# Kernel tuning notes

Hardware: AMD Instinct MI355X
Metric: run time of the kernel (lower is better)

Reference implementation:

```python
import jax, jax.numpy as jnp
import numpy as np

B, C, CO, N = 2, 32, 32, 64
MODES, LMAX, RBINS = 16, 2, 16
HALF = MODES // 2
NL = (LMAX + 1) ** 2  # 9 real spherical harmonics up to l=2
M = MODES ** 3
HID = 16  # round(CO * 0.5)


def _build_basis():
    # frequencies of the kept FNO corner modes along each axis
    f = np.concatenate([np.arange(HALF), np.arange(-HALF, 0)]).astype(np.float32)
    kx, ky, kz = np.meshgrid(f, f, f, indexing='ij')
    kx, ky, kz = kx.ravel(), ky.ravel(), kz.ravel()
    r = np.sqrt(kx ** 2 + ky ** 2 + kz ** 2)
    nzm = (r > 0).astype(np.float32)
    inv = np.where(r > 0, 1.0 / np.maximum(r, 1e-9), 0.0)
    ux, uy, uz = kx * inv, ky * inv, kz * inv
    # real spherical harmonics l=0,1,2 (cartesian form); all l>0 vanish at DC
    Y = np.stack([
        0.282095 * np.ones_like(r),
        0.488603 * uy, 0.488603 * uz, 0.488603 * ux,
        1.092548 * ux * uy, 1.092548 * uy * uz,
        0.315392 * (3.0 * uz ** 2 - nzm),
        1.092548 * ux * uz, 0.546274 * (ux ** 2 - uy ** 2)], axis=0)  # [NL, M]
    shell = np.minimum((r / (r.max() + 1e-6) * RBINS).astype(np.int64), RBINS - 1)
    cnt = np.bincount(shell, minlength=RBINS).astype(np.float32)
    w = 1.0 / np.sqrt(np.maximum(cnt, 1.0))
    mask = (shell[None, :] == np.arange(RBINS)[:, None]).astype(np.float32) * w[:, None]  # [RBINS, M]
    return (mask[:, None, :] * Y[None]).reshape(RBINS * NL, M).astype(np.float32)

BASIS = jnp.asarray(_build_basis())  # [K=144, M=4096], fixed projection basis
IDX = jnp.asarray(np.concatenate([np.arange(HALF), np.arange(N - HALF, N)]))  # kept mode indices


def cgelu(z):
    return jax.nn.gelu(z.real) + 1j * jax.nn.gelu(z.imag)


def setup_inputs() -> dict:
    key = jax.random.key(0)
    ks = jax.random.split(key, 17)
    rn = lambda k, s: jax.random.normal(k, s, dtype=jnp.float32)
    return {
        'x': rn(ks[0], (B, C, N, N, N)),
        'w_fno_r': rn(ks[1], (CO, C)) * 0.1, 'w_fno_i': rn(ks[2], (CO, C)) * 0.1,
        'b_fno_r': rn(ks[3], (CO,)) * 0.1, 'b_fno_i': rn(ks[4], (CO,)) * 0.1,
        'w_gate_r': rn(ks[5], (CO,)), 'w_gate_i': rn(ks[6], (CO,)),
        'w_spec_r': rn(ks[7], (RBINS, NL, C, CO)) * 0.1, 'w_spec_i': rn(ks[8], (RBINS, NL, C, CO)) * 0.1,
        'mlp_w1_r': rn(ks[9], (HID, CO)) * 0.1, 'mlp_w1_i': rn(ks[10], (HID, CO)) * 0.1,
        'mlp_b1_r': rn(ks[11], (HID,)) * 0.1, 'mlp_b1_i': rn(ks[12], (HID,)) * 0.1,
        'mlp_w2_r': rn(ks[13], (CO, HID)) * 0.1, 'mlp_w2_i': rn(ks[14], (CO, HID)) * 0.1,
        'mlp_b2_r': rn(ks[15], (CO,)) * 0.1, 'mlp_b2_i': rn(ks[16], (CO,)) * 0.1,
    }


def reference(x, w_fno_r, w_fno_i, b_fno_r, b_fno_i, w_gate_r, w_gate_i,
              w_spec_r, w_spec_i, mlp_w1_r, mlp_w1_i, mlp_b1_r, mlp_b1_i,
              mlp_w2_r, mlp_w2_i, mlp_b2_r, mlp_b2_i):
    cx = lambda r, i: (r + 1j * i).astype(jnp.complex64)
    xc = x.astype(jnp.complex64)
    w_fno, b_fno = cx(w_fno_r, w_fno_i), cx(b_fno_r, b_fno_i)
    w_gate = cx(w_gate_r, w_gate_i)
    w_spec = cx(w_spec_r, w_spec_i)
    w1, b1 = cx(mlp_w1_r, mlp_w1_i), cx(mlp_b1_r, mlp_b1_i)
    w2, b2 = cx(mlp_w2_r, mlp_w2_i), cx(mlp_b2_r, mlp_b2_i)

    # skip paths: complex 1x1-conv ('linear') and complex soft-gating
    skip_fno = jnp.einsum('oc,bcxyz->boxyz', w_fno, xc) + b_fno[None, :, None, None, None]
    skip_mlp = xc * w_gate[None, :, None, None, None]

    # Harmonic layer: FFT -> slice kept modes -> harmonic/radial projection
    # -> complex spectral conv -> inverse projection -> scatter -> iFFT
    xf = jnp.fft.fftn(xc, axes=(-3, -2, -1))
    xs = xf[:, :, IDX[:, None, None], IDX[None, :, None], IDX[None, None, :]].reshape(B, C, M)
    coeffs = jnp.einsum('bcm,km->bck', xs, BASIS).reshape(B, C, RBINS, NL)
    coeffs = jnp.einsum('bisl,slio->bosl', coeffs, w_spec)
    xs2 = jnp.einsum('bck,km->bcm', coeffs.reshape(B, CO, RBINS * NL), BASIS)
    full = jnp.zeros((B, CO, N, N, N), jnp.complex64).at[
        :, :, IDX[:, None, None], IDX[None, :, None], IDX[None, None, :]
    ].set(xs2.reshape(B, CO, MODES, MODES, MODES))
    x_fno = jnp.fft.ifftn(full, axes=(-3, -2, -1))

    x1 = x_fno + skip_fno  # n_layers=1 -> no activation here
    h = cgelu(jnp.einsum('hc,bcxyz->bhxyz', w1, x1) + b1[None, :, None, None, None])
    y = jnp.einsum('oh,bhxyz->boxyz', w2, h) + b2[None, :, None, None, None]
    return (y + skip_mlp).real
```

## Files before the change

kernel.cpp:

```cpp
#include <hip/hip_runtime.h>
#include <hip/hip_bf16.h>

#define PI2 6.283185307179586f

typedef __attribute__((ext_vector_type(8))) short short8;
typedef __attribute__((ext_vector_type(4))) float f32x4;

static const size_t O_Y      = 0;
static const size_t O_W1RT   = 36864;
static const size_t O_W1IT   = 37376;
static const size_t O_W1XR   = 37888;
static const size_t O_W1XI   = 38400;
static const size_t O_B1PR   = 38912;
static const size_t O_B1PI   = 38928;
static const size_t O_WSH    = 38944;
static const size_t O_SHELL  = 38960;
static const size_t O_ORDER  = 43056;
static const size_t O_SSTART = 47152;
static const size_t O_COEF   = 47232;
static const size_t O_COEF2  = 65664;
static const size_t O_XS     = 84096;
static const size_t O_FRAG   = 608384;
static const size_t O_T2     = 1132672;
static const size_t O_T1     = 3229824;

static __device__ __forceinline__ float geluf(float v) {
  float e = __expf(-1.702f * v);
  return v / (1.0f + e);
}

static __device__ __forceinline__ unsigned int f2bfbits(float f) {
  unsigned int u = __float_as_uint(f);
  u += 0x7fffu + ((u >> 16) & 1u);
  return u >> 16;
}

static __device__ __forceinline__ unsigned int pk2(float a, float b) {
  return f2bfbits(a) | (f2bfbits(b) << 16);
}

__global__ __launch_bounds__(256) void k0_init(
    const float* __restrict__ wfr, const float* __restrict__ wfi,
    const float* __restrict__ bfr, const float* __restrict__ bfi,
    const float* __restrict__ w1r, const float* __restrict__ w1i,
    const float* __restrict__ b1r, const float* __restrict__ b1i,
    const float* __restrict__ w2r, const float* __restrict__ w2i,
    float* __restrict__ ws) {
  float* Y    = ws + O_Y;
  float* w1rt = ws + O_W1RT;  float* w1it = ws + O_W1IT;
  float* W1xr = ws + O_W1XR;  float* W1xi = ws + O_W1XI;
  float* b1pr = ws + O_B1PR;  float* b1pi = ws + O_B1PI;
  float* wsh  = ws + O_WSH;
  int* shellOf = (int*)(ws + O_SHELL);
  int* order   = (int*)(ws + O_ORDER);
  int* sstart  = (int*)(ws + O_SSTART);

  __shared__ int cnt[16], fill[16], st[17];
  int tid = threadIdx.x;
  if (tid < 16) { cnt[tid] = 0; fill[tid] = 0; }
  __syncthreads();
  for (int m = tid; m < 4096; m += 256) {
    int ix = m >> 8, iy = (m >> 4) & 15, iz = m & 15;
    float kx = (float)(ix < 8 ? ix : ix - 16);
    float ky = (float)(iy < 8 ? iy : iy - 16);
    float kz = (float)(iz < 8 ? iz : iz - 16);
    float r2 = kx*kx + ky*ky + kz*kz;
    float r  = sqrtf(r2);
    float nzm = r2 > 0.f ? 1.f : 0.f;
    float inv = r2 > 0.f ? 1.0f / fmaxf(r, 1e-9f) : 0.f;
    float ux = kx*inv, uy = ky*inv, uz = kz*inv;
    Y[0*4096+m] = 0.282095f;
    Y[1*4096+m] = 0.488603f * uy;
    Y[2*4096+m] = 0.488603f * uz;
    Y[3*4096+m] = 0.488603f * ux;
    Y[4*4096+m] = 1.092548f * ux*uy;
    Y[5*4096+m] = 1.092548f * uy*uz;
    Y[6*4096+m] = 0.315392f * (3.0f*uz*uz - nzm);
    Y[7*4096+m] = 1.092548f * ux*uz;
    Y[8*4096+m] = 0.546274f * (ux*ux - uy*uy);
    float rmax = sqrtf(192.0f);
    float t = r / (rmax + 1e-6f) * 16.0f;
    int sh = (int)t; sh = sh > 15 ? 15 : sh;
    shellOf[m] = sh;
    atomicAdd(&cnt[sh], 1);
  }
  __syncthreads();
  if (tid == 0) { int a = 0; for (int s = 0; s < 16; ++s) { st[s] = a; a += cnt[s]; } st[16] = a; }
  __syncthreads();
  if (tid < 16) wsh[tid] = 1.0f / sqrtf(fmaxf((float)cnt[tid], 1.0f));
  if (tid < 17) sstart[tid] = st[tid];
  for (int m = tid; m < 4096; m += 256) {
    int sh = shellOf[m];
    int p = atomicAdd(&fill[sh], 1);
    order[st[sh] + p] = m;
  }
  for (int e = tid; e < 512; e += 256) {
    int j = e >> 5, c = e & 31;
    float ar = 0.f, ai = 0.f;
    for (int o = 0; o < 32; ++o) {
      float wr_ = w1r[j*32+o], wi_ = w1i[j*32+o];
      float fr  = wfr[o*32+c], fi_ = wfi[o*32+c];
      ar += wr_*fr - wi_*fi_;
      ai += wr_*fi_ + wi_*fr;
    }
    W1xr[c*16+j] = ar;  W1xi[c*16+j] = ai;
    w1rt[c*16+j] = w1r[j*32+c];
    w1it[c*16+j] = w1i[j*32+c];
  }
  if (tid < 16) {
    int j = tid;
    float ar = b1r[j], ai = b1i[j];
    for (int o = 0; o < 32; ++o) {
      ar += w1r[j*32+o]*bfr[o] - w1i[j*32+o]*bfi[o];
      ai += w1r[j*32+o]*bfi[o] + w1i[j*32+o]*bfr[o];
    }
    b1pr[j] = ar; b1pi[j] = ai;
  }
  __syncthreads();

  {
    unsigned int* fp = (unsigned int*)(ws + O_FRAG) + tid*32;
    int lane = tid & 63, wvv = tid >> 6;
    int p = lane & 15, q = lane >> 4;
    int z = wvv*16 + p;
    float arj[8], aij[8];
    #pragma unroll
    for (int j = 0; j < 8; ++j) {
      int k = 8*q + j;
      int kz = k & 15;
      float f = (float)(kz < 8 ? kz : kz - 16);
      float s, c; __sincosf(PI2 * f * (float)z / 64.0f, &s, &c);
      arj[j] = (k < 16) ? c : -s;
      aij[j] = (k < 16) ? s : c;
    }
    #pragma unroll
    for (int s2 = 0; s2 < 4; ++s2) {
      fp[s2]     = pk2(arj[2*s2], arj[2*s2+1]);
      fp[4 + s2] = pk2(aij[2*s2], aij[2*s2+1]);
    }
    #pragma unroll
    for (int s = 0; s < 4; ++s) {
      int c0 = 8*q + 2*s, c1 = c0 + 1;
      fp[8  + s] = pk2(w1rt[c0*16 + p], w1rt[c1*16 + p]);
      fp[12 + s] = pk2(w1it[c0*16 + p], w1it[c1*16 + p]);
      fp[16 + s] = pk2(W1xr[c0*16 + p], W1xr[c1*16 + p]);
      fp[20 + s] = pk2(W1xi[c0*16 + p], W1xi[c1*16 + p]);
    }
    #pragma unroll
    for (int mt = 0; mt < 2; ++mt) {
      int o = mt*16 + p;
      #pragma unroll
      for (int s = 0; s < 4; ++s) {
        int kk = 8*q + 2*s;
        float a  = (kk   < 16) ? w2r[o*16 + kk]      : -w2i[o*16 + kk - 16];
        float bb = (kk+1 < 16) ? w2r[o*16 + kk + 1]  : -w2i[o*16 + kk - 15];
        fp[24 + mt*4 + s] = pk2(a, bb);
      }
    }
  }
}

__global__ __launch_bounds__(256) void k12_fwd(const float* __restrict__ x, float* __restrict__ T2) {
  __shared__ __align__(16) float zS[4096];
  __shared__ float2 slab[64*17];
  __shared__ float2 tw[16*17];
  float* zP = zS;  float* zQ = zS + 1024;  float* zB = zS + 2048;  float* zD = zS + 3072;
  float* ysum = zS;
  int blk = blockIdx.x;
  const float* src = x + (size_t)blk * 4096;
  int tid = threadIdx.x;

  {
    int y = tid >> 2, zt = tid & 3;
    const float4* s4 = (const float4*)(src + y*64);
    float4 u0 = s4[zt];
    float4 u1 = s4[zt + 4];
    float4 u2 = s4[zt + 8];
    float4 u3 = s4[zt + 12];
    const float* p0 = (const float*)&u0; const float* p1 = (const float*)&u1;
    const float* p2 = (const float*)&u2; const float* p3 = (const float*)&u3;
    int base = 4*zt*64 + y;
    #pragma unroll
    for (int e = 0; e < 4; ++e) {
      float a = p0[e] + p2[e], c = p1[e] + p3[e];
      float bb = p0[e] - p2[e], d = p1[e] - p3[e];
      zP[base + e*64] = a + c;
      zQ[base + e*64] = a - c;
      zB[base + e*64] = bb;
      zD[base + e*64] = d;
    }
  }
  {
    int k = tid >> 4, i2 = tid & 15;
    float f = (float)(k < 8 ? k : k - 16);
    float ang = -PI2 * f * (float)i2 / 64.0f;
    float sw, cw; __sincosf(ang, &sw, &cw);
    tw[k*17 + i2] = make_float2(cw, sw);
  }
  __syncthreads();

  {
    int kz = tid & 15, yq = tid >> 4;
    int j = kz & 3;
    const float2* twp = tw + kz*17;
    float arr[4] = {0.f,0.f,0.f,0.f}, aii[4] = {0.f,0.f,0.f,0.f};
    if ((j & 1) == 0) {
      const float* plane = (j == 0) ? zP : zQ;
      #pragma unroll
      for (int z0 = 0; z0 < 16; ++z0) {
        float2 w = twp[z0];
        float4 s = *(const float4*)&plane[z0*64 + 4*yq];
        arr[0] += s.x*w.x; aii[0] += s.x*w.y;
        arr[1] += s.y*w.x; aii[1] += s.y*w.y;
        arr[2] += s.z*w.x; aii[2] += s.z*w.y;
        arr[3] += s.w*w.x; aii[3] += s.w*w.y;
      }
    } else {
      float dsg = (j == 1) ? -1.f : 1.f;
      #pragma unroll
      for (int z0 = 0; z0 < 16; ++z0) {
        float2 w = twp[z0];
        float4 b = *(const float4*)&zB[z0*64 + 4*yq];
        float4 d = *(const float4*)&zD[z0*64 + 4*yq];
        float swi = dsg * w.y, swr = dsg * w.x;
        arr[0] += b.x*w.x - d.x*swi;  aii[0] += b.x*w.y + d.x*swr;
        arr[1] += b.y*w.x - d.y*swi;  aii[1] += b.y*w.y + d.y*swr;
        arr[2] += b.z*w.x - d.z*swi;  aii[2] += b.z*w.y + d.z*swr;
        arr[3] += b.w*w.x - d.w*swi;  aii[3] += b.w*w.y + d.w*swr;
      }
    }
    int y0 = 4*yq;
    slab[(y0+0)*17 + kz] = make_float2(arr[0], aii[0]);
    slab[(y0+1)*17 + kz] = make_float2(arr[1], aii[1]);
    slab[(y0+2)*17 + kz] = make_float2(arr[2], aii[2]);
    slab[(y0+3)*17 + kz] = make_float2(arr[3], aii[3]);
  }
  __syncthreads();

  {
    int y0 = tid >> 4, kz = tid & 15;
    float2 u0 = slab[(y0     )*17 + kz];
    float2 u1 = slab[(y0 + 16)*17 + kz];
    float2 u2 = slab[(y0 + 32)*17 + kz];
    float2 u3 = slab[(y0 + 48)*17 + kz];
    float Ar = u0.x + u2.x, Ai = u0.y + u2.y;
    float Br = u0.x - u2.x, Bi = u0.y - u2.y;
    float Cr = u1.x + u3.x, Ci = u1.y + u3.y;
    float Dr = u1.x - u3.x, Di = u1.y - u3.y;
    float* yp = ysum + y0*162 + kz*10;
    yp[0] = Ar + Cr;  yp[1] = Ai + Ci;
    yp[2] = Br + Di;  yp[3] = Bi - Dr;
    yp[4] = Ar - Cr;  yp[5] = Ai - Ci;
    yp[6] = Br - Di;  yp[7] = Bi + Dr;
  }
  __syncthreads();

  {
    int kz = tid & 15, kyi = tid >> 4;
    const float* yp = ysum + kz*10 + (kyi & 3)*2;
    const float2* twp = tw + kyi*17;
    float ar = 0.f, ai = 0.f;
    #pragma unroll
    for (int y0 = 0; y0 < 16; ++y0) {
      float sr = yp[y0*162], si = yp[y0*162 + 1];
      float2 w = twp[y0];
      ar += sr*w.x - si*w.y;
      ai += sr*w.y + si*w.x;
    }
    *(float2*)&T2[(size_t)blk*512 + (kyi*16 + kz)*2] = make_float2(ar, ai);
  }
}

__global__ __launch_bounds__(256) void k3_dftx(const float* __restrict__ T2, float* __restrict__ xs) {
  __shared__ float slab[64*34];
  __shared__ float xsum[2592];
  __shared__ float2 twx[16*17];
  int blk = blockIdx.x;
  int bc = blk >> 4, ky = blk & 15;
  int tid = threadIdx.x;
  for (int i = tid; i < 2048; i += 256) {
    int xr = i >> 5, rem = i & 31;
    slab[xr*34 + rem] = T2[((size_t)(bc*64 + xr)*16 + ky)*32 + rem];
  }
  {
    int k = tid >> 4, i2 = tid & 15;
    float f = (float)(k < 8 ? k : k - 16);
    float ang = -PI2 * f * (float)i2 / 64.0f;
    float sw, cw; __sincosf(ang, &sw, &cw);
    twx[k*17 + i2] = make_float2(cw, sw);
  }
  __syncthreads();
  {
    int x0 = tid >> 4, kz = tid & 15;
    const float2* sp = (const float2*)slab;
    float2 u0 = sp[(x0     )*17 + kz];
    float2 u1 = sp[(x0 + 16)*17 + kz];
    float2 u2 = sp[(x0 + 32)*17 + kz];
    float2 u3 = sp[(x0 + 48)*17 + kz];
    float Ar = u0.x + u2.x, Ai = u0.y + u2.y;
    float Br = u0.x - u2.x, Bi = u0.y - u2.y;
    float Cr = u1.x + u3.x, Ci = u1.y + u3.y;
    float Dr = u1.x - u3.x, Di = u1.y - u3.y;
    float* yp = xsum + x0*162 + kz*10;
    yp[0] = Ar + Cr;  yp[1] = Ai + Ci;
    yp[2] = Br + Di;  yp[3] = Bi - Dr;
    yp[4] = Ar - Cr;  yp[5] = Ai - Ci;
    yp[6] = Br - Di;  yp[7] = Bi + Dr;
  }
  __syncthreads();
  {
    int kz = tid & 15, kxi = tid >> 4;
    const float* yp = xsum + kz*10 + (kxi & 3)*2;
    const float2* twp = twx + kxi*17;
    float ar = 0.f, ai = 0.f;
    #pragma unroll
    for (int x0 = 0; x0 < 16; ++x0) {
      float sr = yp[x0*162], si = yp[x0*162 + 1];
      float2 w = twp[x0];
      ar += sr*w.x - si*w.y;
      ai += sr*w.y + si*w.x;
    }
    *(float2*)&xs[(size_t)bc*8192 + (kxi*256 + ky*16 + kz)*2] = make_float2(ar, ai);
  }
}

__global__ __launch_bounds__(256) void k4_proj(const float* __restrict__ xs, const float* __restrict__ Y,
    const int* __restrict__ order, const int* __restrict__ sstart, const float* __restrict__ wsh,
    float* __restrict__ coeffs) {
  int blk = blockIdx.x; int bc = blk >> 4, s = blk & 15;
  int tid = threadIdx.x;
  int st = sstart[s], en = sstart[s+1];
  float ar[9], ai[9];
  #pragma unroll
  for (int l = 0; l < 9; ++l) { ar[l] = 0.f; ai[l] = 0.f; }
  for (int ii = st + tid; ii < en; ii += 256) {
    int m = order[ii];
    float2 v = *(const float2*)&xs[(size_t)bc*8192 + m*2];
    #pragma unroll
    for (int l = 0; l < 9; ++l) {
      float yv = Y[l*4096 + m];
      ar[l] += yv * v.x; ai[l] += yv * v.y;
    }
  }
  #pragma unroll
  for (int l = 0; l < 9; ++l) {
    #pragma unroll
    for (int d = 1; d < 64; d <<= 1) {
      ar[l] += __shfl_xor(ar[l], d, 64);
      ai[l] += __shfl_xor(ai[l], d, 64);
    }
  }
  __shared__ float wred[4][18];
  int wv = tid >> 6, lane = tid & 63;
  if (lane == 0) {
    #pragma unroll
    for (int l = 0; l < 9; ++l) { wred[wv][l] = ar[l]; wred[wv][9 + l] = ai[l]; }
  }
  __syncthreads();
  if (tid < 18) {
    float sum = wred[0][tid] + wred[1][tid] + wred[2][tid] + wred[3][tid];
    float w = wsh[s];
    int l = tid < 9 ? tid : tid - 9;
    int ri = tid < 9 ? 0 : 1;
    coeffs[((size_t)bc*144 + s*9 + l)*2 + ri] = w * sum;
  }
}

__global__ __launch_bounds__(256) void k5_spec(const float* __restrict__ coeffs,
    const float* __restrict__ wsr, const float* __restrict__ wsi, float* __restrict__ coeffs2) {
  int item = blockIdx.x * 8 + (threadIdx.x >> 5);
  int b = item / 144, sl = item - b * 144;
  int o = threadIdx.x & 31;
  float ar = 0.f, ai = 0.f;
  for (int i = 0; i < 32; ++i) {
    float cr = coeffs[((size_t)(b*32 + i)*144 + sl)*2];
    float ci = coeffs[((size_t)(b*32 + i)*144 + sl)*2 + 1];
    float wr = wsr[(sl*32 + i)*32 + o];
    float wi = wsi[(sl*32 + i)*32 + o];
    ar += cr*wr - ci*wi;
    ai += cr*wi + ci*wr;
  }
  const float sc = 1.0f / 262144.0f;
  coeffs2[((size_t)(b*32 + o)*144 + sl)*2]     = ar * sc;
  coeffs2[((size_t)(b*32 + o)*144 + sl)*2 + 1] = ai * sc;
}

__global__ __launch_bounds__(256) void k78(const float* __restrict__ coeffs2,
    const float* __restrict__ Y, const int* __restrict__ shellOf, const float* __restrict__ wsh,
    float* __restrict__ U1) {
  __shared__ float c2[288];
  __shared__ float slab[512];
  int blk = blockIdx.x;
  int bo = blk >> 4, ky = blk & 15;
  int tid = threadIdx.x;

  for (int i = tid; i < 288; i += 256) c2[i] = coeffs2[(size_t)bo*288 + i];
  __syncthreads();

  {
    int kxi = tid >> 4, kz = tid & 15;
    int m = kxi*256 + ky*16 + kz;
    int sh = shellOf[m];
    float w = wsh[sh];
    float ar = 0.f, ai = 0.f;
    #pragma unroll
    for (int l = 0; l < 9; ++l) {
      float yv = Y[l*4096 + m];
      ar += yv * c2[(sh*9 + l)*2];
      ai += yv * c2[(sh*9 + l)*2 + 1];
    }
    slab[tid*2]     = w * ar;
    slab[tid*2 + 1] = w * ai;
  }
  __syncthreads();

  int kz = tid & 15, grp = tid >> 4;
  float ang = PI2 * (float)grp / 64.0f;
  float sw, cw; __sincosf(ang, &sw, &cw);
  float tr = 1.f, ti = 0.f;
  float sjr[4] = {0.f,0.f,0.f,0.f}, sji[4] = {0.f,0.f,0.f,0.f};
  #pragma unroll
  for (int kx = 0; kx < 16; ++kx) {
    if (kx == 8) ti = -ti;
    float2 v = *(const float2*)&slab[(kx*16 + kz)*2];
    sjr[kx & 3] += v.x*tr - v.y*ti;
    sji[kx & 3] += v.x*ti + v.y*tr;
    float nt = tr*cw - ti*sw; ti = tr*sw + ti*cw; tr = nt;
  }
  float Ar = sjr[0]+sjr[2], Ai = sji[0]+sji[2];
  float Br = sjr[0]-sjr[2], Bi = sji[0]-sji[2];
  float Cr = sjr[1]+sjr[3], Ci = sji[1]+sji[3];
  float Dr = sjr[1]-sjr[3], Di = sji[1]-sji[3];
  *(float2*)&U1[((size_t)(bo*64 + grp     )*16 + ky)*32 + kz*2] = make_float2(Ar+Cr, Ai+Ci);
  *(float2*)&U1[((size_t)(bo*64 + grp + 16)*16 + ky)*32 + kz*2] = make_float2(Br-Di, Bi+Dr);
  *(float2*)&U1[((size_t)(bo*64 + grp + 32)*16 + ky)*32 + kz*2] = make_float2(Ar-Cr, Ai-Ci);
  *(float2*)&U1[((size_t)(bo*64 + grp + 48)*16 + ky)*32 + kz*2] = make_float2(Br+Di, Bi-Dr);
}

__global__ __launch_bounds__(256) void k9_invy(const float* __restrict__ U1, float* __restrict__ U2) {
  __shared__ float slab[512];
  int blk = blockIdx.x;
  int tid = threadIdx.x;
  const float* src = U1 + (size_t)blk * 512;
  for (int i = tid; i < 512; i += 256) slab[i] = src[i];
  __syncthreads();
  int kz = tid & 15, grp = tid >> 4;
  float ang = PI2 * (float)grp / 64.0f;
  float sw, cw; __sincosf(ang, &sw, &cw);
  float tr = 1.f, ti = 0.f;
  float sjr[4] = {0.f,0.f,0.f,0.f}, sji[4] = {0.f,0.f,0.f,0.f};
  #pragma unroll
  for (int ky = 0; ky < 16; ++ky) {
    if (ky == 8) ti = -ti;
    float2 v = *(const float2*)&slab[(ky*16 + kz)*2];
    sjr[ky & 3] += v.x*tr - v.y*ti;
    sji[ky & 3] += v.x*ti + v.y*tr;
    float nt = tr*cw - ti*sw; ti = tr*sw + ti*cw; tr = nt;
  }
  float Ar = sjr[0]+sjr[2], Ai = sji[0]+sji[2];
  float Br = sjr[0]-sjr[2], Bi = sji[0]-sji[2];
  float Cr = sjr[1]+sjr[3], Ci = sji[1]+sji[3];
  float Dr = sjr[1]-sjr[3], Di = sji[1]-sji[3];
  float* dst = U2 + (size_t)blk * 2048;
  *(float2*)&dst[((grp     )*16 + kz)*2] = make_float2(Ar+Cr, Ai+Ci);
  *(float2*)&dst[((grp + 16)*16 + kz)*2] = make_float2(Br-Di, Bi+Dr);
  *(float2*)&dst[((grp + 32)*16 + kz)*2] = make_float2(Ar-Cr, Ai-Ci);
  *(float2*)&dst[((grp + 48)*16 + kz)*2] = make_float2(Br+Di, Bi-Dr);
}

__global__ __launch_bounds__(256) void k10_final(
    const float* __restrict__ x, const float* __restrict__ U2,
    const float* __restrict__ ws,
    const float* __restrict__ b2r, const float* __restrict__ wgr,
    float* __restrict__ out) {
  const float* b1pr = ws + O_B1PR;  const float* b1pi = ws + O_B1PI;

  __shared__ unsigned int xfT[128*33];
  __shared__ __hip_bfloat16 xlT[128*34];
  __shared__ f32x4 hpW4[272];
  unsigned int* hpW = (unsigned int*)hpW4;
  unsigned int* Bt  = (unsigned int*)hpW4;

  int tid = threadIdx.x;
  int blk = blockIdx.x;
  int yb = blk & 31, bx = blk >> 5;
  int b = bx >> 6, xr = bx & 63;
  int y0 = yb * 2;

  int lane = tid & 63, wv = tid >> 6;
  int p = lane & 15, q = lane >> 4;

  union U8 { short8 v; unsigned int u[4]; };

  const uint4* fpt = (const uint4*)(ws + O_FRAG) + (size_t)tid * 8;
  U8 fAr, fAi;
  {
    uint4 a0 = fpt[0], a1 = fpt[1];
    fAr.u[0]=a0.x; fAr.u[1]=a0.y; fAr.u[2]=a0.z; fAr.u[3]=a0.w;
    fAi.u[0]=a1.x; fAi.u[1]=a1.y; fAi.u[2]=a1.z; fAi.u[3]=a1.w;
  }

  for (int i = tid; i < 1024; i += 256) {
    int ya = i >> 9, c = (i >> 4) & 31, zq = i & 15;
    const float4 v = *(const float4*)&x[(size_t)(b*32 + c)*262144 + (size_t)xr*4096
                                        + (size_t)(y0 + ya)*64 + 4*zq];
    int rb = ((ya << 6) + 4*zq)*34 + c;
    xlT[rb]       = __float2bfloat16(v.x);
    xlT[rb + 34]  = __float2bfloat16(v.y);
    xlT[rb + 68]  = __float2bfloat16(v.z);
    xlT[rb + 102] = __float2bfloat16(v.w);
  }
  {
    int ya = tid >> 7, o = (tid >> 2) & 31, t4 = tid & 3;
    const float4* g4 = (const float4*)(U2 + ((size_t)((b*32 + o)*64 + xr))*2048
                                       + (size_t)(y0 + ya)*32 + 8*t4);
    float4 ga = g4[0], gb = g4[1];
    unsigned int* bp = Bt + (ya*32 + o)*17;
    bp[2*t4]         = pk2(ga.x, ga.z);
    bp[2*t4 + 1]     = pk2(gb.x, gb.z);
    bp[8 + 2*t4]     = pk2(ga.y, ga.w);
    bp[8 + 2*t4 + 1] = pk2(gb.y, gb.w);
  }
  __syncthreads();

  {
    f32x4 zac = {0.f, 0.f, 0.f, 0.f};
    #pragma unroll
    for (int ya = 0; ya < 2; ++ya) {
      #pragma unroll
      for (int ot = 0; ot < 2; ++ot) {
        U8 fB;
        uint4 bv = *(const uint4*)(Bt + (ya*32 + ot*16 + p)*17 + 4*q);
        fB.u[0] = bv.x; fB.u[1] = bv.y; fB.u[2] = bv.z; fB.u[3] = bv.w;
        f32x4 Dr = __builtin_amdgcn_mfma_f32_16x16x32_bf16(fAr.v, fB.v, zac, 0, 0, 0);
        f32x4 Di = __builtin_amdgcn_mfma_f32_16x16x32_bf16(fAi.v, fB.v, zac, 0, 0, 0);
        int rowb = ya*64 + wv*16 + 4*q;
        #pragma unroll
        for (int r = 0; r < 4; ++r)
          xfT[(rowb + r)*33 + ot*16 + p] = pk2(Dr[r], Di[r]);
      }
    }
  }
  __syncthreads();

  {
    int wb = wv * 272;

    U8 fW1r, fW1i, fW1iN, fW1xr, fW1xi, fW2[2];
    {
      uint4 b0 = fpt[2], b1 = fpt[3], b2v = fpt[4], b3 = fpt[5], b4 = fpt[6], b5 = fpt[7];
      fW1r.u[0]=b0.x;  fW1r.u[1]=b0.y;  fW1r.u[2]=b0.z;  fW1r.u[3]=b0.w;
      fW1i.u[0]=b1.x;  fW1i.u[1]=b1.y;  fW1i.u[2]=b1.z;  fW1i.u[3]=b1.w;
      fW1xr.u[0]=b2v.x; fW1xr.u[1]=b2v.y; fW1xr.u[2]=b2v.z; fW1xr.u[3]=b2v.w;
      fW1xi.u[0]=b3.x; fW1xi.u[1]=b3.y; fW1xi.u[2]=b3.z; fW1xi.u[3]=b3.w;
      fW2[0].u[0]=b4.x; fW2[0].u[1]=b4.y; fW2[0].u[2]=b4.z; fW2[0].u[3]=b4.w;
      fW2[1].u[0]=b5.x; fW2[1].u[1]=b5.y; fW2[1].u[2]=b5.z; fW2[1].u[3]=b5.w;
      #pragma unroll
      for (int s = 0; s < 4; ++s) fW1iN.u[s] = fW1i.u[s] ^ 0x80008000u;
    }
    float4 b1r4 = *(const float4*)(b1pr + 4*q);
    float4 b1i4 = *(const float4*)(b1pi + 4*q);
    float b2a[2][4], wga[2][4];
    #pragma unroll
    for (int mt = 0; mt < 2; ++mt) {
      float4 t0 = *(const float4*)(b2r + mt*16 + 4*q);
      float4 t1 = *(const float4*)(wgr + mt*16 + 4*q);
      b2a[mt][0]=t0.x; b2a[mt][1]=t0.y; b2a[mt][2]=t0.z; b2a[mt][3]=t0.w;
      wga[mt][0]=t1.x; wga[mt][1]=t1.y; wga[mt][2]=t1.z; wga[mt][3]=t1.w;
    }
    float b1ra[4] = {b1r4.x, b1r4.y, b1r4.z, b1r4.w};
    float b1ia[4] = {b1i4.x, b1i4.y, b1i4.z, b1i4.w};

    f32x4 zacc = {0.f, 0.f, 0.f, 0.f};
    const unsigned int* xlW = (const unsigned int*)xlT;

    for (int tt = 0; tt < 2; ++tt) {
      int tile = wv*2 + tt;
      int ya = tile >> 2, zg = tile & 3;
      int row = ya*64 + zg*16 + p;

      unsigned int w8[8];
      #pragma unroll
      for (int jj = 0; jj < 8; ++jj) w8[jj] = xfT[row*33 + 8*q + jj];
      U8 FR, FI, XV;
      #pragma unroll
      for (int s = 0; s < 4; ++s) {
        FR.u[s] = __builtin_amdgcn_perm(w8[2*s+1], w8[2*s], 0x05040100u);
        FI.u[s] = __builtin_amdgcn_perm(w8[2*s+1], w8[2*s], 0x07060302u);
        XV.u[s] = xlW[row*17 + 4*q + s];
      }

      f32x4 accR = zacc, accI = zacc;
      accR = __builtin_amdgcn_mfma_f32_16x16x32_bf16(fW1r.v,  FR.v, accR, 0, 0, 0);
      accR = __builtin_amdgcn_mfma_f32_16x16x32_bf16(fW1iN.v, FI.v, accR, 0, 0, 0);
      accR = __builtin_amdgcn_mfma_f32_16x16x32_bf16(fW1xr.v, XV.v, accR, 0, 0, 0);
      accI = __builtin_amdgcn_mfma_f32_16x16x32_bf16(fW1r.v,  FI.v, accI, 0, 0, 0);
      accI = __builtin_amdgcn_mfma_f32_16x16x32_bf16(fW1i.v,  FR.v, accI, 0, 0, 0);
      accI = __builtin_amdgcn_mfma_f32_16x16x32_bf16(fW1xi.v, XV.v, accI, 0, 0, 0);

      float hr_[4], hi_[4];
      #pragma unroll
      for (int r = 0; r < 4; ++r) {
        hr_[r] = geluf(accR[r] + b1ra[r]);
        hi_[r] = geluf(accI[r] + b1ia[r]);
      }
      hpW[wb + 17*p + 2*q]     = pk2(hr_[0], hr_[1]);
      hpW[wb + 17*p + 2*q + 1] = pk2(hr_[2], hr_[3]);
      hpW[wb + 17*p + 8 + 2*q]     = pk2(hi_[0], hi_[1]);
      hpW[wb + 17*p + 8 + 2*q + 1] = pk2(hi_[2], hi_[3]);

      U8 FH;
      #pragma unroll
      for (int s = 0; s < 4; ++s) FH.u[s] = hpW[wb + 17*p + 4*q + s];

      #pragma unroll
      for (int mt = 0; mt < 2; ++mt) {
        f32x4 accO = __builtin_amdgcn_mfma_f32_16x16x32_bf16(fW2[mt].v, FH.v, zacc, 0, 0, 0);
        #pragma unroll
        for (int r = 0; r < 4; ++r) {
          int o = mt*16 + q*4 + r;
          int z = zg*16 + p;
          float xv = __bfloat162float(xlT[row*34 + o]);
          out[(size_t)(b*32 + o)*262144 + (size_t)xr*4096 + (size_t)(y0 + ya)*64 + z]
              = accO[r] + b2a[mt][r] + wga[mt][r]*xv;
        }
      }
    }
  }
}

extern "C" void kernel_launch(void* const* d_in, const int* in_sizes, int n_in,
                              void* d_out, int out_size, void* d_ws, size_t ws_size,
                              hipStream_t stream) {
  (void)in_sizes; (void)n_in; (void)out_size; (void)ws_size;
  const float* x   = (const float*)d_in[0];
  const float* wfr = (const float*)d_in[1];
  const float* wfi = (const float*)d_in[2];
  const float* bfr = (const float*)d_in[3];
  const float* bfi = (const float*)d_in[4];
  const float* wgr = (const float*)d_in[5];
  const float* wsr = (const float*)d_in[7];
  const float* wsi = (const float*)d_in[8];
  const float* w1r = (const float*)d_in[9];
  const float* w1i = (const float*)d_in[10];
  const float* b1r = (const float*)d_in[11];
  const float* b1i = (const float*)d_in[12];
  const float* w2r = (const float*)d_in[13];
  const float* w2i = (const float*)d_in[14];
  const float* b2r = (const float*)d_in[15];
  float* out = (float*)d_out;
  float* ws  = (float*)d_ws;

  float* T1      = ws + O_T1;
  float* T2      = ws + O_T2;
  float* xs      = ws + O_XS;
  float* coeffs  = ws + O_COEF;
  float* coeffs2 = ws + O_COEF2;
  float* Y       = ws + O_Y;
  int* shellOf   = (int*)(ws + O_SHELL);
  int* order     = (int*)(ws + O_ORDER);
  int* sstart    = (int*)(ws + O_SSTART);
  float* wsh     = ws + O_WSH;

  hipLaunchKernelGGL(k0_init,  dim3(1),    dim3(256), 0, stream, wfr, wfi, bfr, bfi, w1r, w1i, b1r, b1i, w2r, w2i, ws);
  hipLaunchKernelGGL(k12_fwd,  dim3(4096), dim3(256), 0, stream, x, T2);
  hipLaunchKernelGGL(k3_dftx,  dim3(1024), dim3(256), 0, stream, T2, xs);
  hipLaunchKernelGGL(k4_proj,  dim3(1024), dim3(256), 0, stream, xs, Y, order, sstart, wsh, coeffs);
  hipLaunchKernelGGL(k5_spec,  dim3(36),   dim3(256), 0, stream, coeffs, wsr, wsi, coeffs2);
  hipLaunchKernelGGL(k78,      dim3(1024), dim3(256), 0, stream, coeffs2, Y, shellOf, wsh, T2);
  hipLaunchKernelGGL(k9_invy,  dim3(4096), dim3(256), 0, stream, T2, T1);
  hipLaunchKernelGGL(k10_final,dim3(4096), dim3(256), 0, stream, x, T1, ws, b2r, wgr, out);
}
```

Baseline: 248.4 us.

## Compute forward z-DFT with bf16 MFMA and precompute twiddle tables

```diff
diff --git a/kernel.cpp b/kernel.cpp
--- a/kernel.cpp
+++ b/kernel.cpp
@@ -21,6 +21,9 @@
 static const size_t O_COEF2  = 65664;
 static const size_t O_XS     = 84096;
 static const size_t O_FRAG   = 608384;
+static const size_t O_TWF    = 616576;
+static const size_t O_TWB    = 617088;
+static const size_t O_FRG12  = 617600;
 static const size_t O_T2     = 1132672;
 static const size_t O_T1     = 3229824;
 
@@ -116,6 +119,38 @@
     }
     b1pr[j] = ar; b1pi[j] = ai;
   }
+
+  {
+    int k = tid >> 4, i2 = tid & 15;
+    float fk = (float)(k < 8 ? k : k - 16);
+    float s, c;
+    __sincosf(-PI2 * fk * (float)i2 / 64.0f, &s, &c);
+    ((float2*)(ws + O_TWF))[tid] = make_float2(c, s);
+    int g = tid >> 4, kk = tid & 15;
+    float fkk = (float)(kk < 8 ? kk : kk - 16);
+    __sincosf(PI2 * fkk * (float)g / 64.0f, &s, &c);
+    ((float2*)(ws + O_TWB))[tid] = make_float2(c, s);
+  }
+  if (tid < 64) {
+    unsigned int* fp12 = (unsigned int*)(ws + O_FRG12) + tid*16;
+    int p = tid & 15, q = tid >> 4;
+    float fp_ = (float)(p < 8 ? p : p - 16);
+    #pragma unroll
+    for (int ch = 0; ch < 2; ++ch) {
+      float cj[8], sj[8];
+      #pragma unroll
+      for (int j = 0; j < 8; ++j) {
+        int z = ch*32 + 8*q + j;
+        float s, c; __sincosf(-PI2 * fp_ * (float)z / 64.0f, &s, &c);
+        cj[j] = c; sj[j] = s;
+      }
+      #pragma unroll
+      for (int s2 = 0; s2 < 4; ++s2) {
+        fp12[ch*8 + s2]     = pk2(cj[2*s2], cj[2*s2+1]);
+        fp12[ch*8 + 4 + s2] = pk2(sj[2*s2], sj[2*s2+1]);
+      }
+    }
+  }
   __syncthreads();
 
   {
@@ -160,80 +195,55 @@
   }
 }
 
-__global__ __launch_bounds__(256) void k12_fwd(const float* __restrict__ x, float* __restrict__ T2) {
-  __shared__ __align__(16) float zS[4096];
+__global__ __launch_bounds__(256) void k12_fwd(const float* __restrict__ x,
+    const float* __restrict__ ws, float* __restrict__ T2) {
+  __shared__ __align__(16) float us[2592];
   __shared__ float2 slab[64*17];
-  __shared__ float2 tw[16*17];
-  float* zP = zS;  float* zQ = zS + 1024;  float* zB = zS + 2048;  float* zD = zS + 3072;
-  float* ysum = zS;
+  __hip_bfloat16* xT = (__hip_bfloat16*)us;
+  float* ysum = us;
   int blk = blockIdx.x;
   const float* src = x + (size_t)blk * 4096;
   int tid = threadIdx.x;
-
-  {
-    int y = tid >> 2, zt = tid & 3;
-    const float4* s4 = (const float4*)(src + y*64);
-    float4 u0 = s4[zt];
-    float4 u1 = s4[zt + 4];
-    float4 u2 = s4[zt + 8];
-    float4 u3 = s4[zt + 12];
-    const float* p0 = (const float*)&u0; const float* p1 = (const float*)&u1;
-    const float* p2 = (const float*)&u2; const float* p3 = (const float*)&u3;
-    int base = 4*zt*64 + y;
-    #pragma unroll
-    for (int e = 0; e < 4; ++e) {
-      float a = p0[e] + p2[e], c = p1[e] + p3[e];
-      float bb = p0[e] - p2[e], d = p1[e] - p3[e];
-      zP[base + e*64] = a + c;
-      zQ[base + e*64] = a - c;
-      zB[base + e*64] = bb;
-      zD[base + e*64] = d;
-    }
-  }
-  {
-    int k = tid >> 4, i2 = tid & 15;
-    float f = (float)(k < 8 ? k : k - 16);
-    float ang = -PI2 * f * (float)i2 / 64.0f;
-    float sw, cw; __sincosf(ang, &sw, &cw);
-    tw[k*17 + i2] = make_float2(cw, sw);
-  }
-  __syncthreads();
-
-  {
-    int kz = tid & 15, yq = tid >> 4;
-    int j = kz & 3;
-    const float2* twp = tw + kz*17;
-    float arr[4] = {0.f,0.f,0.f,0.f}, aii[4] = {0.f,0.f,0.f,0.f};
-    if ((j & 1) == 0) {
-      const float* plane = (j == 0) ? zP : zQ;
-      #pragma unroll
-      for (int z0 = 0; z0 < 16; ++z0) {
-        float2 w = twp[z0];
-        float4 s = *(const float4*)&plane[z0*64 + 4*yq];
-        arr[0] += s.x*w.x; aii[0] += s.x*w.y;
-        arr[1] += s.y*w.x; aii[1] += s.y*w.y;
-        arr[2] += s.z*w.x; aii[2] += s.z*w.y;
-        arr[3] += s.w*w.x; aii[3] += s.w*w.y;
-      }
-    } else {
-      float dsg = (j == 1) ? -1.f : 1.f;
-      #pragma unroll
-      for (int z0 = 0; z0 < 16; ++z0) {
-        float2 w = twp[z0];
-        float4 b = *(const float4*)&zB[z0*64 + 4*yq];
-        float4 d = *(const float4*)&zD[z0*64 + 4*yq];
-        float swi = dsg * w.y, swr = dsg * w.x;
-        arr[0] += b.x*w.x - d.x*swi;  aii[0] += b.x*w.y + d.x*swr;
-        arr[1] += b.y*w.x - d.y*swi;  aii[1] += b.y*w.y + d.y*swr;
-        arr[2] += b.z*w.x - d.z*swi;  aii[2] += b.z*w.y + d.z*swr;
-        arr[3] += b.w*w.x - d.w*swi;  aii[3] += b.w*w.y + d.w*swr;
-      }
-    }
-    int y0 = 4*yq;
-    slab[(y0+0)*17 + kz] = make_float2(arr[0], aii[0]);
-    slab[(y0+1)*17 + kz] = make_float2(arr[1], aii[1]);
-    slab[(y0+2)*17 + kz] = make_float2(arr[2], aii[2]);
-    slab[(y0+3)*17 + kz] = make_float2(arr[3], aii[3]);
+  int lane = tid & 63, wv = tid >> 6;
+  int p = lane & 15, q = lane >> 4;
+
+  union U8 { short8 v; unsigned int u[4]; };
+
+  U8 fc0, fs0, fc1, fs1;
+  {
+    const uint4* f12 = (const uint4*)(ws + O_FRG12) + (size_t)lane*4;
+    uint4 a0 = f12[0], a1 = f12[1], a2 = f12[2], a3 = f12[3];
+    fc0.u[0]=a0.x; fc0.u[1]=a0.y; fc0.u[2]=a0.z; fc0.u[3]=a0.w;
+    fs0.u[0]=a1.x; fs0.u[1]=a1.y; fs0.u[2]=a1.z; fs0.u[3]=a1.w;
+    fc1.u[0]=a2.x; fc1.u[1]=a2.y; fc1.u[2]=a2.z; fc1.u[3]=a2.w;
+    fs1.u[0]=a3.x; fs1.u[1]=a3.y; fs1.u[2]=a3.z; fs1.u[3]=a3.w;
+  }
+
+  for (int i = tid; i < 1024; i += 256) {
+    int y = i >> 4, zq = i & 15;
+    float4 v = *(const float4*)&src[y*64 + 4*zq];
+    int rb = y*72 + 4*zq;
+    xT[rb]   = __float2bfloat16(v.x);
+    xT[rb+1] = __float2bfloat16(v.y);
+    xT[rb+2] = __float2bfloat16(v.z);
+    xT[rb+3] = __float2bfloat16(v.w);
+  }
+  __syncthreads();
+
+  {
+    U8 b0, b1;
+    const __hip_bfloat16* xrow = &xT[(wv*16 + p)*72];
+    *(uint4*)&b0.u[0] = *(const uint4*)&xrow[8*q];
+    *(uint4*)&b1.u[0] = *(const uint4*)&xrow[32 + 8*q];
+    f32x4 zac = {0.f, 0.f, 0.f, 0.f};
+    f32x4 Dr = __builtin_amdgcn_mfma_f32_16x16x32_bf16(fc0.v, b0.v, zac, 0, 0, 0);
+    Dr       = __builtin_amdgcn_mfma_f32_16x16x32_bf16(fc1.v, b1.v, Dr,  0, 0, 0);
+    f32x4 Di = __builtin_amdgcn_mfma_f32_16x16x32_bf16(fs0.v, b0.v, zac, 0, 0, 0);
+    Di       = __builtin_amdgcn_mfma_f32_16x16x32_bf16(fs1.v, b1.v, Di,  0, 0, 0);
+    __syncthreads();
+    #pragma unroll
+    for (int r = 0; r < 4; ++r)
+      slab[(wv*16 + p)*17 + 4*q + r] = make_float2(Dr[r], Di[r]);
   }
   __syncthreads();
 
@@ -258,7 +268,7 @@
   {
     int kz = tid & 15, kyi = tid >> 4;
     const float* yp = ysum + kz*10 + (kyi & 3)*2;
-    const float2* twp = tw + kyi*17;
+    const float2* twp = (const float2*)(ws + O_TWF) + kyi*16;
     float ar = 0.f, ai = 0.f;
     #pragma unroll
     for (int y0 = 0; y0 < 16; ++y0) {
@@ -271,23 +281,16 @@
   }
 }
 
-__global__ __launch_bounds__(256) void k3_dftx(const float* __restrict__ T2, float* __restrict__ xs) {
+__global__ __launch_bounds__(256) void k3_dftx(const float* __restrict__ T2,
+    const float* __restrict__ ws, float* __restrict__ xs) {
   __shared__ float slab[64*34];
   __shared__ float xsum[2592];
-  __shared__ float2 twx[16*17];
   int blk = blockIdx.x;
   int bc = blk >> 4, ky = blk & 15;
   int tid = threadIdx.x;
   for (int i = tid; i < 2048; i += 256) {
     int xr = i >> 5, rem = i & 31;
     slab[xr*34 + rem] = T2[((size_t)(bc*64 + xr)*16 + ky)*32 + rem];
-  }
-  {
-    int k = tid >> 4, i2 = tid & 15;
-    float f = (float)(k < 8 ? k : k - 16);
-    float ang = -PI2 * f * (float)i2 / 64.0f;
-    float sw, cw; __sincosf(ang, &sw, &cw);
-    twx[k*17 + i2] = make_float2(cw, sw);
   }
   __syncthreads();
   {
@@ -311,7 +314,7 @@
   {
     int kz = tid & 15, kxi = tid >> 4;
     const float* yp = xsum + kz*10 + (kxi & 3)*2;
-    const float2* twp = twx + kxi*17;
+    const float2* twp = (const float2*)(ws + O_TWF) + kxi*16;
     float ar = 0.f, ai = 0.f;
     #pragma unroll
     for (int x0 = 0; x0 < 16; ++x0) {
@@ -387,7 +390,7 @@
 
 __global__ __launch_bounds__(256) void k78(const float* __restrict__ coeffs2,
     const float* __restrict__ Y, const int* __restrict__ shellOf, const float* __restrict__ wsh,
-    float* __restrict__ U1) {
+    const float* __restrict__ twb, float* __restrict__ U1) {
   __shared__ float c2[288];
   __shared__ float slab[512];
   int blk = blockIdx.x;
@@ -415,17 +418,14 @@
   __syncthreads();
 
   int kz = tid & 15, grp = tid >> 4;
-  float ang = PI2 * (float)grp / 64.0f;
-  float sw, cw; __sincosf(ang, &sw, &cw);
-  float tr = 1.f, ti = 0.f;
+  const float2* tb = (const float2*)twb + grp*16;
   float sjr[4] = {0.f,0.f,0.f,0.f}, sji[4] = {0.f,0.f,0.f,0.f};
   #pragma unroll
   for (int kx = 0; kx < 16; ++kx) {
-    if (kx == 8) ti = -ti;
+    float2 w = tb[kx];
     float2 v = *(const float2*)&slab[(kx*16 + kz)*2];
-    sjr[kx & 3] += v.x*tr - v.y*ti;
-    sji[kx & 3] += v.x*ti + v.y*tr;
-    float nt = tr*cw - ti*sw; ti = tr*sw + ti*cw; tr = nt;
+    sjr[kx & 3] += v.x*w.x - v.y*w.y;
+    sji[kx & 3] += v.x*w.y + v.y*w.x;
   }
   float Ar = sjr[0]+sjr[2], Ai = sji[0]+sji[2];
   float Br = sjr[0]-sjr[2], Bi = sji[0]-sji[2];
@@ -437,7 +437,8 @@
   *(float2*)&U1[((size_t)(bo*64 + grp + 48)*16 + ky)*32 + kz*2] = make_float2(Br+Di, Bi-Dr);
 }
 
-__global__ __launch_bounds__(256) void k9_invy(const float* __restrict__ U1, float* __restrict__ U2) {
+__global__ __launch_bounds__(256) void k9_invy(const float* __restrict__ U1,
+    const float* __restrict__ twb, float* __restrict__ U2) {
   __shared__ float slab[512];
   int blk = blockIdx.x;
   int tid = threadIdx.x;
@@ -445,17 +446,14 @@
   for (int i = tid; i < 512; i += 256) slab[i] = src[i];
   __syncthreads();
   int kz = tid & 15, grp = tid >> 4;
-  float ang = PI2 * (float)grp / 64.0f;
-  float sw, cw; __sincosf(ang, &sw, &cw);
-  float tr = 1.f, ti = 0.f;
+  const float2* tb = (const float2*)twb + grp*16;
   float sjr[4] = {0.f,0.f,0.f,0.f}, sji[4] = {0.f,0.f,0.f,0.f};
   #pragma unroll
   for (int ky = 0; ky < 16; ++ky) {
-    if (ky == 8) ti = -ti;
+    float2 w = tb[ky];
     float2 v = *(const float2*)&slab[(ky*16 + kz)*2];
-    sjr[ky & 3] += v.x*tr - v.y*ti;
-    sji[ky & 3] += v.x*ti + v.y*tr;
-    float nt = tr*cw - ti*sw; ti = tr*sw + ti*cw; tr = nt;
+    sjr[ky & 3] += v.x*w.x - v.y*w.y;
+    sji[ky & 3] += v.x*w.y + v.y*w.x;
   }
   float Ar = sjr[0]+sjr[2], Ai = sji[0]+sji[2];
   float Br = sjr[0]-sjr[2], Bi = sji[0]-sji[2];
@@ -661,13 +659,14 @@
   int* order     = (int*)(ws + O_ORDER);
   int* sstart    = (int*)(ws + O_SSTART);
   float* wsh     = ws + O_WSH;
+  float* twb     = ws + O_TWB;
 
   hipLaunchKernelGGL(k0_init,  dim3(1),    dim3(256), 0, stream, wfr, wfi, bfr, bfi, w1r, w1i, b1r, b1i, w2r, w2i, ws);
-  hipLaunchKernelGGL(k12_fwd,  dim3(4096), dim3(256), 0, stream, x, T2);
-  hipLaunchKernelGGL(k3_dftx,  dim3(1024), dim3(256), 0, stream, T2, xs);
+  hipLaunchKernelGGL(k12_fwd,  dim3(4096), dim3(256), 0, stream, x, ws, T2);
+  hipLaunchKernelGGL(k3_dftx,  dim3(1024), dim3(256), 0, stream, T2, ws, xs);
   hipLaunchKernelGGL(k4_proj,  dim3(1024), dim3(256), 0, stream, xs, Y, order, sstart, wsh, coeffs);
   hipLaunchKernelGGL(k5_spec,  dim3(36),   dim3(256), 0, stream, coeffs, wsr, wsi, coeffs2);
-  hipLaunchKernelGGL(k78,      dim3(1024), dim3(256), 0, stream, coeffs2, Y, shellOf, wsh, T2);
-  hipLaunchKernelGGL(k9_invy,  dim3(4096), dim3(256), 0, stream, T2, T1);
+  hipLaunchKernelGGL(k78,      dim3(1024), dim3(256), 0, stream, coeffs2, Y, shellOf, wsh, twb, T2);
+  hipLaunchKernelGGL(k9_invy,  dim3(4096), dim3(256), 0, stream, T2, twb, T1);
   hipLaunchKernelGGL(k10_final,dim3(4096), dim3(256), 0, stream, x, T1, ws, b2r, wgr, out);
 }
```

Measured after the change: 238.3 us (median of 2 runs). 4.1% less time.
